# Kernel tuning notes

Hardware: AMD Instinct MI355X
Metric: run time of the kernel (lower is better)

Reference implementation:

```python
import jax, jax.numpy as jnp
import numpy as np

N = 128  # image size
J = 4    # number of scales
L = 4    # number of orientations


def make_morlet_filters(n, j_max, n_angles):
    """Fixed Morlet filter bank in Fourier space, shape [J, L, N, N] (real)."""
    freqs = np.fft.fftfreq(n) * 2.0 * np.pi
    kx = freqs[:, None] * np.ones((1, n))
    ky = np.ones((n, 1)) * freqs[None, :]
    filters = np.zeros((j_max, n_angles, n, n), dtype=np.float32)
    for j in range(j_max):
        k0 = 3.0 * np.pi / 4.0 / (2.0 ** j)   # central frequency of scale j
        sigma = 0.8 * (2.0 ** j)               # gaussian width in space
        for l in range(n_angles):
            theta = np.pi * l / n_angles
            k0x, k0y = k0 * np.cos(theta), k0 * np.sin(theta)
            beta = np.exp(-0.5 * sigma ** 2 * k0 ** 2)  # zero-mean correction
            g_shift = np.exp(-0.5 * sigma ** 2 * ((kx - k0x) ** 2 + (ky - k0y) ** 2))
            g_zero = np.exp(-0.5 * sigma ** 2 * (kx ** 2 + ky ** 2))
            filters[j, l] = g_shift - beta * g_zero
    return jnp.asarray(filters)


PSI = make_morlet_filters(N, J, L)  # fixed (non-learned) filter bank
VALID_PAIRS = [(j1, j2) for j1 in range(J) for j2 in range(J) if j2 > j1]  # 6 pairs


def setup_inputs() -> dict:
    key = jax.random.key(0)
    k1, k2, k3, k4, k5 = jax.random.split(key, 5)
    B = 64
    return {
        "image_batch": jax.random.normal(k1, (B, N, N), dtype=jnp.float32),
        "fc1_w": jax.random.normal(k2, (4, 11), dtype=jnp.float32) * 0.3,
        "fc1_b": jax.random.normal(k3, (4,), dtype=jnp.float32) * 0.1,
        "fc2_w": jax.random.normal(k4, (10, 4), dtype=jnp.float32) * 0.3,
        "fc2_b": jax.random.normal(k5, (10,), dtype=jnp.float32) * 0.1,
    }


def _scattering(image):
    # image: [B, N, N]
    i_hat = jnp.fft.fft2(image)  # [B,N,N] complex64
    s0 = jnp.mean(image, axis=(1, 2))  # [B]
    # first order: |x * psi_{j1,l1}|  -> [B,J,L,N,N]
    u1 = jnp.abs(jnp.fft.ifft2(i_hat[:, None, None] * PSI[None]))
    s1 = jnp.mean(u1, axis=(2, 3, 4))  # [B,J] averaged over orientations+space
    u1_hat = jnp.fft.fft2(u1)  # [B,J,L,N,N]
    # second order: only j2 > j1 (others NaN in original and masked out)
    s2_list = []
    for (j1, j2) in VALID_PAIRS:
        # [B, L1, L2, N, N]
        field = jnp.fft.ifft2(u1_hat[:, j1, :, None] * PSI[j2][None, None])
        s2_list.append(jnp.mean(jnp.abs(field), axis=(1, 2, 3, 4)))
    s2 = jnp.stack(s2_list, axis=1)  # [B,6]
    return jnp.concatenate([s0[:, None], s1, s2], axis=1)  # [B,11]


def reference(image_batch, fc1_w, fc1_b, fc2_w, fc2_b):
    coeffs = _scattering(image_batch)                      # [B,11]
    h = jax.nn.relu(coeffs @ fc1_w.T + fc1_b)              # [B,4]
    return jax.nn.sigmoid(h @ fc2_w.T + fc2_b)             # [B,10]
```

## Files before the change

### kernel.cpp

```cpp
#include <hip/hip_runtime.h>
#include <math.h>

#define NN   128
#define SS   129
#define TT   512
#define NPIX 16384
#define EPT  32
#define SG   65
#define SG32 33


__device__ __forceinline__ float2 cmul(float2 a, float2 w) {
    return make_float2(a.x * w.x - a.y * w.y, a.x * w.y + a.y * w.x);
}
__device__ __forceinline__ float2 cmulc(float2 a, float2 w) {
    return make_float2(a.x * w.x + a.y * w.y, a.y * w.x - a.x * w.y);
}

template<int SGN>
__device__ __forceinline__ void fft4(float2* f) {
    float2 t0 = make_float2(f[0].x + f[2].x, f[0].y + f[2].y);
    float2 t1 = make_float2(f[0].x - f[2].x, f[0].y - f[2].y);
    float2 t2 = make_float2(f[1].x + f[3].x, f[1].y + f[3].y);
    float2 t3 = make_float2(f[1].x - f[3].x, f[1].y - f[3].y);
    float2 t3i = (SGN > 0) ? make_float2(-t3.y, t3.x) : make_float2(t3.y, -t3.x);
    f[0] = make_float2(t0.x + t2.x, t0.y + t2.y);
    f[1] = make_float2(t1.x + t3i.x, t1.y + t3i.y);
    f[2] = make_float2(t0.x - t2.x, t0.y - t2.y);
    f[3] = make_float2(t1.x - t3i.x, t1.y - t3i.y);
}

template<int SGN>
__device__ __forceinline__ void fft8(float2* f) {
    const float R = 0.70710678118654752f;
    const float WC[4] = {1.f, R, 0.f, -R};
    const float WS[4] = {0.f, R, 1.f, R};
    #pragma unroll
    for (int stage = 0; stage < 3; ++stage) {
        const int L = 8 >> stage, half = L >> 1, step = 1 << stage;
        #pragma unroll
        for (int base = 0; base < 8; base += L) {
            #pragma unroll
            for (int j = 0; j < half; ++j) {
                float2 u = f[base + j], v = f[base + half + j];
                f[base + j] = make_float2(u.x + v.x, u.y + v.y);
                float dx = u.x - v.x, dy = u.y - v.y;
                const int t = j * step;
                const float wr = WC[t];
                const float wi = (SGN > 0) ? WS[t] : -WS[t];
                f[base + half + j] = make_float2(dx * wr - dy * wi, dx * wi + dy * wr);
            }
        }
    }
    float2 tmp;
    tmp = f[1]; f[1] = f[4]; f[4] = tmp;
    tmp = f[3]; f[3] = f[6]; f[6] = tmp;
}

template<int SGN>
__device__ __forceinline__ void fft16(float2* f) {
    const float WC[8] = {1.f, 0.92387953251f, 0.70710678119f, 0.38268343236f,
                         0.f, -0.38268343236f, -0.70710678119f, -0.92387953251f};
    const float WS[8] = {0.f, 0.38268343236f, 0.70710678119f, 0.92387953251f,
                         1.f, 0.92387953251f, 0.70710678119f, 0.38268343236f};
    #pragma unroll
    for (int stage = 0; stage < 4; ++stage) {
        const int L = 16 >> stage, half = L >> 1, step = 1 << stage;
        #pragma unroll
        for (int base = 0; base < 16; base += L) {
            #pragma unroll
            for (int j = 0; j < half; ++j) {
                float2 u = f[base + j], v = f[base + half + j];
                f[base + j] = make_float2(u.x + v.x, u.y + v.y);
                float dx = u.x - v.x, dy = u.y - v.y;
                const int t = j * step;
                const float wr = WC[t];
                const float wi = (SGN > 0) ? WS[t] : -WS[t];
                f[base + half + j] = make_float2(dx * wr - dy * wi, dx * wi + dy * wr);
            }
        }
    }
    float2 tmp;
    tmp = f[1];  f[1]  = f[8];  f[8]  = tmp;
    tmp = f[2];  f[2]  = f[4];  f[4]  = tmp;
    tmp = f[3];  f[3]  = f[12]; f[12] = tmp;
    tmp = f[5];  f[5]  = f[10]; f[10] = tmp;
    tmp = f[7];  f[7]  = f[14]; f[14] = tmp;
    tmp = f[11]; f[11] = f[13]; f[13] = tmp;
}

__device__ __forceinline__ float waveReduceSum(float v) {
    #pragma unroll
    for (int off = 32; off > 0; off >>= 1) v += __shfl_down(v, off, 64);
    return v;
}

__device__ __forceinline__ void buildTw(float2* tw, int tid) {
    if (tid < 128) {
        float s, c;
        __sincosf((float)tid * 0.04908738521234052f, &s, &c);
        tw[tid] = make_float2(c, s);
    }
}

template<int ES, int LS>
__device__ __forceinline__ void fwdA(float2* __restrict__ F,
                                     const float2* __restrict__ tw, int tid) {
    #pragma unroll
    for (int i = 0; i < 4; ++i) {
        int u = i * TT + tid;
        int t = u >> 7, x = u & 127;
        float2* M = F + x * LS;
        float2 f[8];
        #pragma unroll
        for (int n1 = 0; n1 < 8; ++n1) f[n1] = M[(t + 16 * n1) * ES];
        fft8<-1>(f);
        #pragma unroll
        for (int ka = 0; ka < 8; ++ka)
            M[(t + 16 * ka) * ES] = cmulc(f[ka], tw[t * ka]);
    }
}

template<int ES, int LS>
__device__ __forceinline__ void fwdB(float2* __restrict__ F, int tid) {
    #pragma unroll
    for (int i = 0; i < 2; ++i) {
        int u = i * TT + tid;
        int ka = u >> 7, x = u & 127;
        float2* M = F + x * LS;
        float2 g[16];
        #pragma unroll
        for (int t = 0; t < 16; ++t) g[t] = M[(16 * ka + t) * ES];
        fft16<-1>(g);
        #pragma unroll
        for (int kb = 0; kb < 16; ++kb) M[(16 * ka + kb) * ES] = g[kb];
    }
}

__device__ __forceinline__ void fwdB_col_capture(const float2* __restrict__ F, int tid,
                                                 float2* __restrict__ uh) {
    #pragma unroll
    for (int i = 0; i < 2; ++i) {
        int u = i * TT + tid;
        int ka = u >> 7, c = u & 127;
        float2 g[16];
        #pragma unroll
        for (int t = 0; t < 16; ++t) g[t] = F[(16 * ka + t) * SS + c];
        fft16<-1>(g);
        #pragma unroll
        for (int kb = 0; kb < 16; ++kb) uh[i * 16 + kb] = g[kb];
    }
}

template<int ES, int LS>
__device__ __forceinline__ void invA(float2* __restrict__ F,
                                     const float2* __restrict__ tw, int tid) {
    #pragma unroll
    for (int i = 0; i < 2; ++i) {
        int u = i * TT + tid;
        int ka = u >> 7, x = u & 127;
        float2* M = F + x * LS;
        float2 g[16];
        #pragma unroll
        for (int kb = 0; kb < 16; ++kb) g[kb] = M[(16 * ka + kb) * ES];
        fft16<1>(g);
        #pragma unroll
        for (int t = 0; t < 16; ++t)
            M[(16 * ka + t) * ES] = cmul(g[t], tw[t * ka]);
    }
}

template<int ES, int LS>
__device__ __forceinline__ void invB(float2* __restrict__ F, int tid) {
    #pragma unroll
    for (int i = 0; i < 4; ++i) {
        int u = i * TT + tid;
        int t = u >> 7, x = u & 127;
        float2* M = F + x * LS;
        float2 f[8];
        #pragma unroll
        for (int ka = 0; ka < 8; ++ka) f[ka] = M[(16 * ka + t) * ES];
        fft8<1>(f);
        #pragma unroll
        for (int nh = 0; nh < 8; ++nh) M[(t + 16 * nh) * ES] = f[nh];
    }
}

__device__ __forceinline__ void invBmag_fwdA_row(float2* __restrict__ F,
                                                 const float2* __restrict__ tw,
                                                 int tid, float& acc) {
    #pragma unroll
    for (int i = 0; i < 4; ++i) {
        int u = i * TT + tid;
        int t = u >> 7, x = u & 127;
        float2* M = F + x * SS;
        float2 f[8];
        #pragma unroll
        for (int ka = 0; ka < 8; ++ka) f[ka] = M[16 * ka + t];
        fft8<1>(f);
        #pragma unroll
        for (int nh = 0; nh < 8; ++nh) {
            float m = sqrtf(f[nh].x * f[nh].x + f[nh].y * f[nh].y);
            acc += m;
            f[nh] = make_float2(m, 0.f);
        }
        fft8<-1>(f);
        #pragma unroll
        for (int ka = 0; ka < 8; ++ka)
            M[t + 16 * ka] = cmulc(f[ka], tw[t * ka]);
    }
}

__global__ __attribute__((amdgpu_flat_work_group_size(TT, TT), amdgpu_waves_per_eu(2, 2)))
void k_pre(const float* __restrict__ img,
           float* __restrict__ psi,
           float2* __restrict__ ihat,
           float* __restrict__ coeffs) {
    __shared__ float2 F[NN * SS];
    __shared__ float2 tw[128];
    __shared__ float red[TT / 64];
    int blk = blockIdx.x, tid = threadIdx.x;
    if (blk >= 64) {
        if (blk == 80) {
            for (int i = tid; i < 64 * 11; i += TT)
                if (i % 11 != 0) coeffs[i] = 0.f;
            return;
        }
        int f = blk - 64;
        int j = f >> 2, l = f & 3;
        float k0    = 2.35619449019234493f / (float)(1 << j);
        float sigma = 0.8f * (float)(1 << j);
        float s2    = sigma * sigma;
        float theta = 0.78539816339744831f * (float)l;
        float k0x = k0 * cosf(theta);
        float k0y = k0 * sinf(theta);
        float beta = expf(-0.5f * s2 * k0 * k0);
        const float FSTEP = 0.04908738521234052f;
        float* dst = psi + (size_t)f * NPIX;
        for (int i = tid; i < NPIX; i += TT) {
            int pr = i >> 7, pc = i & 127;
            int kr = (pr >> 4) + 8 * (pr & 15);
            int kc = (pc >> 4) + 8 * (pc & 15);
            float fr = (float)(kr < 64 ? kr : kr - 128) * FSTEP;
            float fc = (float)(kc < 64 ? kc : kc - 128) * FSTEP;
            float dx = fr - k0x, dy = fc - k0y;
            float g1 = expf(-0.5f * s2 * (dx * dx + dy * dy));
            float g0 = expf(-0.5f * s2 * (fr * fr + fc * fc));
            dst[i] = g1 - beta * g0;
        }
        return;
    }
    int b = blk;
    buildTw(tw, tid);
    const float* im = img + (size_t)b * NPIX;
    float acc = 0.f;
    #pragma unroll
    for (int k = 0; k < EPT; ++k) {
        int e = k * TT + tid;
        float v = im[e];
        acc += v;
        F[(e >> 7) * SS + (e & 127)] = make_float2(v, 0.f);
    }
    float ws = waveReduceSum(acc);
    if ((tid & 63) == 0) red[tid >> 6] = ws;
    __syncthreads();
    if (tid == 0) {
        float t = 0.f;
        #pragma unroll
        for (int w = 0; w < TT / 64; ++w) t += red[w];
        coeffs[b * 11 + 0] = t * (1.f / 16384.f);
    }
    fwdA<1, SS>(F, tw, tid);  __syncthreads();
    fwdB<1, SS>(F, tid);      __syncthreads();
    fwdA<SS, 1>(F, tw, tid);  __syncthreads();
    float2 uh[32];
    fwdB_col_capture(F, tid, uh);
    float2* dst = ihat + (size_t)b * NPIX;
    #pragma unroll
    for (int i = 0; i < 2; ++i) {
        int u = i * TT + tid;
        int ka = u >> 7, c = u & 127;
        #pragma unroll
        for (int kb = 0; kb < 16; ++kb)
            dst[(16 * ka + kb) * NN + c] = uh[i * 16 + kb];
    }
}

__global__ __attribute__((amdgpu_flat_work_group_size(TT, TT), amdgpu_waves_per_eu(2, 2)))
void k_scat_big(const float2* __restrict__ ihat,
                const float* __restrict__ psi,
                float* __restrict__ coeffs) {
    __shared__ __align__(16) float2 F[16640];
    __shared__ float2 tw[128];
    float4* G4a = (float4*)F;
    float4* G4b = (float4*)(F + 8320);
    float2* G2a = F;
    float2* G2b = F + 4160;
    float2* G2c = F + 8320;
    float2* G2d = F + 12480;
    int tid = threadIdx.x;
    int x = blockIdx.x;
    int b = x & 63, l1 = x >> 6;
    const float2* ih = ihat + (size_t)b * NPIX;
    const float*  p1 = psi + (size_t)l1 * NPIX;
    buildTw(tw, tid);

    const float S1_128 = 9.3132257461547852e-10f;
    const float S2TR   = 5.6843418860808015e-14f;

    int kalo = tid >> 7, c = tid & 127;
    {
        #pragma unroll
        for (int i = 0; i < 2; ++i) {
            int ka = kalo + 4 * i;
            float2 g[16];
            #pragma unroll
            for (int kb = 0; kb < 16; ++kb) {
                int e = (16 * ka + kb) * NN + c;
                float2 z = ih[e];
                float  p = p1[e];
                g[kb] = make_float2(z.x * p, z.y * p);
            }
            fft16<1>(g);
            #pragma unroll
            for (int t = 0; t < 16; ++t)
                F[(16 * ka + t) * SS + c] = cmul(g[t], tw[t * ka]);
        }
    }
    __syncthreads();
    invB<SS, 1>(F, tid);      __syncthreads();
    invA<1, SS>(F, tw, tid);  __syncthreads();
    float acc = 0.f;
    invBmag_fwdA_row(F, tw, tid, acc);
    float ws1 = waveReduceSum(acc);
    if ((tid & 63) == 0) atomicAdd(&coeffs[b * 11 + 1], ws1 * S1_128);
    __syncthreads();
    fwdB<1, SS>(F, tid);      __syncthreads();
    fwdA<SS, 1>(F, tw, tid);  __syncthreads();
    float2 uh[32];
    fwdB_col_capture(F, tid, uh);
    __syncthreads();

    int m = c & 15;
    bool colKeep = (m < 4) || (m >= 12);
    int pc64 = 8 * (c >> 4) + ((m < 4) ? m : (m - 8));

    {
        const int ORW[4] = {21, 15, 0, -15};
        const int OCW[4] = { 0, 15, 21,  15};
        int fc = (c >> 4) + 8 * (c & 15);
        bool ckw[4]; int pcw[4];
        #pragma unroll
        for (int w = 0; w < 4; ++w) {
            int dc = (fc - OCW[w]) & 127;
            ckw[w] = (dc < 32) || (dc >= 96);
            int uc = (dc < 32) ? dc : (dc - 64);
            pcw[w] = 8 * (uc & 7) + (uc >> 3);
        }
        #pragma unroll
        for (int i = 0; i < 2; ++i) {
            int ka = kalo + 4 * i;
            #pragma unroll
            for (int kb = 0; kb < 16; ++kb) {
                int fr = ka + 8 * kb;
                float2 z = uh[i * 16 + kb];
                int e = (16 * ka + kb) * NN + c;
                #pragma unroll
                for (int w = 0; w < 4; ++w) {
                    if (ckw[w]) {
                        int dr = (fr - ORW[w]) & 127;
                        if (dr < 32 || dr >= 96) {
                            int ur = (dr < 32) ? dr : (dr - 64);
                            int pr = 8 * (ur & 7) + (ur >> 3);
                            float pv = psi[(size_t)(4 + w) * NPIX + e];
                            float2* G = (w == 0) ? G2a : (w == 1) ? G2b
                                       : (w == 2) ? G2c : G2d;
                            G[pr * SG + pcw[w]] = make_float2(z.x * pv, z.y * pv);
                        }
                    }
                }
            }
        }
        __syncthreads();
        {
            int col = tid & 63, k8 = tid >> 6;
            float2 f0[8], f1[8], f2[8], f3[8];
            #pragma unroll
            for (int kb = 0; kb < 8; ++kb) {
                int o = (8 * k8 + kb) * SG + col;
                f0[kb] = G2a[o]; f1[kb] = G2b[o]; f2[kb] = G2c[o]; f3[kb] = G2d[o];
            }
            fft8<1>(f0); fft8<1>(f1); fft8<1>(f2); fft8<1>(f3);
            #pragma unroll
            for (int q = 0; q < 8; ++q) {
                float2 w = tw[2 * q * k8];
                int o = (8 * k8 + q) * SG + col;
                G2a[o] = cmul(f0[q], w); G2b[o] = cmul(f1[q], w);
                G2c[o] = cmul(f2[q], w); G2d[o] = cmul(f3[q], w);
            }
        }
        __syncthreads();
        {
            int col = tid & 63, q = tid >> 6;
            float2 f0[8], f1[8], f2[8], f3[8];
            #pragma unroll
            for (int k8 = 0; k8 < 8; ++k8) {
                int o = (8 * k8 + q) * SG + col;
                f0[k8] = G2a[o]; f1[k8] = G2b[o]; f2[k8] = G2c[o]; f3[k8] = G2d[o];
            }
            fft8<1>(f0); fft8<1>(f1); fft8<1>(f2); fft8<1>(f3);
            #pragma unroll
            for (int n1 = 0; n1 < 8; ++n1) {
                int o = (8 * n1 + q) * SG + col;
                G2a[o] = f0[n1]; G2b[o] = f1[n1]; G2c[o] = f2[n1]; G2d[o] = f3[n1];
            }
        }
        __syncthreads();
        {
            int row = tid & 63, k8 = tid >> 6;
            int base = row * SG + 8 * k8;
            float2 f0[8], f1[8], f2[8], f3[8];
            #pragma unroll
            for (int kb = 0; kb < 8; ++kb) {
                f0[kb] = G2a[base + kb]; f1[kb] = G2b[base + kb];
                f2[kb] = G2c[base + kb]; f3[kb] = G2d[base + kb];
            }
            fft8<1>(f0); fft8<1>(f1); fft8<1>(f2); fft8<1>(f3);
            #pragma unroll
            for (int q = 0; q < 8; ++q) {
                float2 w = tw[2 * q * k8];
                G2a[base + q] = cmul(f0[q], w); G2b[base + q] = cmul(f1[q], w);
                G2c[base + q] = cmul(f2[q], w); G2d[base + q] = cmul(f3[q], w);
            }
        }
        __syncthreads();
        float a2 = 0.f;
        {
            int row = tid & 63, q = tid >> 6;
            int base = row * SG + q;
            float2 f0[8], f1[8], f2[8], f3[8];
            #pragma unroll
            for (int k8 = 0; k8 < 8; ++k8) {
                int o = base + 8 * k8;
                f0[k8] = G2a[o]; f1[k8] = G2b[o]; f2[k8] = G2c[o]; f3[k8] = G2d[o];
            }
            fft8<1>(f0); fft8<1>(f1); fft8<1>(f2); fft8<1>(f3);
            #pragma unroll
            for (int n1 = 0; n1 < 8; ++n1) {
                a2 += sqrtf(f0[n1].x * f0[n1].x + f0[n1].y * f0[n1].y);
                a2 += sqrtf(f1[n1].x * f1[n1].x + f1[n1].y * f1[n1].y);
                a2 += sqrtf(f2[n1].x * f2[n1].x + f2[n1].y * f2[n1].y);
                a2 += sqrtf(f3[n1].x * f3[n1].x + f3[n1].y * f3[n1].y);
            }
        }
        float ws2 = waveReduceSum(a2);
        if ((tid & 63) == 0) atomicAdd(&coeffs[b * 11 + 5 + 0], ws2 * S2TR);
        __syncthreads();
    }

    for (int j2 = 2; j2 <= 3; ++j2) {
        int pair = j2 - 1;
        const float* p0 = psi + (size_t)(j2 * 4 + 0) * NPIX;
        const float* pq1 = p0 + NPIX;
        const float* pq2 = pq1 + NPIX;
        const float* pq3 = pq2 + NPIX;
        if (colKeep) {
            #pragma unroll
            for (int i = 0; i < 2; ++i) {
                int ka = kalo + 4 * i;
                #pragma unroll
                for (int kb = 0; kb < 16; ++kb) {
                    if (kb < 4 || kb >= 12) {
                        int pr64 = 8 * ka + ((kb < 4) ? kb : (kb - 8));
                        float2 z = uh[i * 16 + kb];
                        int e = (16 * ka + kb) * NN + c;
                        float a0 = p0[e], a1 = pq1[e], a2f = pq2[e], a3 = pq3[e];
                        G4a[pr64 * SG + pc64] =
                            make_float4(z.x * a0, z.y * a0, z.x * a1, z.y * a1);
                        G4b[pr64 * SG + pc64] =
                            make_float4(z.x * a2f, z.y * a2f, z.x * a3, z.y * a3);
                    }
                }
            }
        }
        __syncthreads();
        {
            int col = tid & 63, k8 = tid >> 6;
            float2 f0[8], f1[8], f2[8], f3[8];
            #pragma unroll
            for (int kb = 0; kb < 8; ++kb) {
                int o = (8 * k8 + kb) * SG + col;
                float4 v = G4a[o];
                f0[kb] = make_float2(v.x, v.y); f1[kb] = make_float2(v.z, v.w);
                float4 u = G4b[o];
                f2[kb] = make_float2(u.x, u.y); f3[kb] = make_float2(u.z, u.w);
            }
            fft8<1>(f0); fft8<1>(f1); fft8<1>(f2); fft8<1>(f3);
            #pragma unroll
            for (int q = 0; q < 8; ++q) {
                float2 w = tw[2 * q * k8];
                int o = (8 * k8 + q) * SG + col;
                float2 a = cmul(f0[q], w), d = cmul(f1[q], w);
                G4a[o] = make_float4(a.x, a.y, d.x, d.y);
                float2 a2c = cmul(f2[q], w), d2 = cmul(f3[q], w);
                G4b[o] = make_float4(a2c.x, a2c.y, d2.x, d2.y);
            }
        }
        __syncthreads();
        {
            int col = tid & 63, q = tid >> 6;
            float2 f0[8], f1[8], f2[8], f3[8];
            #pragma unroll
            for (int k8 = 0; k8 < 8; ++k8) {
                int o = (8 * k8 + q) * SG + col;
                float4 v = G4a[o];
                f0[k8] = make_float2(v.x, v.y); f1[k8] = make_float2(v.z, v.w);
                float4 u = G4b[o];
                f2[k8] = make_float2(u.x, u.y); f3[k8] = make_float2(u.z, u.w);
            }
            fft8<1>(f0); fft8<1>(f1); fft8<1>(f2); fft8<1>(f3);
            #pragma unroll
            for (int n1 = 0; n1 < 8; ++n1) {
                int o = (8 * n1 + q) * SG + col;
                G4a[o] = make_float4(f0[n1].x, f0[n1].y, f1[n1].x, f1[n1].y);
                G4b[o] = make_float4(f2[n1].x, f2[n1].y, f3[n1].x, f3[n1].y);
            }
        }
        __syncthreads();
        {
            int row = tid & 63, k8 = tid >> 6;
            int base = row * SG + 8 * k8;
            float2 f0[8], f1[8], f2[8], f3[8];
            #pragma unroll
            for (int kb = 0; kb < 8; ++kb) {
                float4 v = G4a[base + kb];
                f0[kb] = make_float2(v.x, v.y); f1[kb] = make_float2(v.z, v.w);
                float4 u = G4b[base + kb];
                f2[kb] = make_float2(u.x, u.y); f3[kb] = make_float2(u.z, u.w);
            }
            fft8<1>(f0); fft8<1>(f1); fft8<1>(f2); fft8<1>(f3);
            #pragma unroll
            for (int q = 0; q < 8; ++q) {
                float2 w = tw[2 * q * k8];
                float2 a = cmul(f0[q], w), d = cmul(f1[q], w);
                G4a[base + q] = make_float4(a.x, a.y, d.x, d.y);
                float2 a2c = cmul(f2[q], w), d2 = cmul(f3[q], w);
                G4b[base + q] = make_float4(a2c.x, a2c.y, d2.x, d2.y);
            }
        }
        __syncthreads();
        float a2 = 0.f;
        {
            int row = tid & 63, q = tid >> 6;
            int base = row * SG + q;
            float2 f0[8], f1[8], f2[8], f3[8];
            #pragma unroll
            for (int k8 = 0; k8 < 8; ++k8) {
                float4 v = G4a[base + 8 * k8];
                f0[k8] = make_float2(v.x, v.y); f1[k8] = make_float2(v.z, v.w);
                float4 u = G4b[base + 8 * k8];
                f2[k8] = make_float2(u.x, u.y); f3[k8] = make_float2(u.z, u.w);
            }
            fft8<1>(f0); fft8<1>(f1); fft8<1>(f2); fft8<1>(f3);
            #pragma unroll
            for (int n1 = 0; n1 < 8; ++n1) {
                a2 += sqrtf(f0[n1].x * f0[n1].x + f0[n1].y * f0[n1].y);
                a2 += sqrtf(f1[n1].x * f1[n1].x + f1[n1].y * f1[n1].y);
                a2 += sqrtf(f2[n1].x * f2[n1].x + f2[n1].y * f2[n1].y);
                a2 += sqrtf(f3[n1].x * f3[n1].x + f3[n1].y * f3[n1].y);
            }
        }
        float ws2 = waveReduceSum(a2);
        if ((tid & 63) == 0) atomicAdd(&coeffs[b * 11 + 5 + pair], ws2 * S2TR);
        __syncthreads();
    }
}

__global__ __attribute__((amdgpu_flat_work_group_size(TT, TT), amdgpu_waves_per_eu(4, 4)))
void k_scat_small(const float2* __restrict__ ihat,
                  const float* __restrict__ psi,
                  float* __restrict__ coeffs) {
    __shared__ __align__(16) float2 S[8320];
    __shared__ float2 tw[128];
    float2* G2  = S;
    float2* G32 = S;
    float4* G32p = (float4*)S;
    float4* G4  = (float4*)S;
    float2* H32 = S + 4160;
    int tid = threadIdx.x;
    int x = blockIdx.x;
    int b = x & 63, l1 = (x >> 6) & 3;
    int t0 = x >> 8;
    int j1 = (t0 == 0) ? 1 : (t0 + 1);
    const float2* ih = ihat + (size_t)b * NPIX;
    const float*  p1 = psi + (size_t)(j1 * 4 + l1) * NPIX;
    buildTw(tw, tid);

    const float S1_64 = 3.7252902984619141e-9f;
    const float S1_32 = 1.4901161193847656e-8f;
    const float S2_32 = 9.0949470177292824e-13f;
    const float S2_V  = 2.2737367544323206e-13f;

    int kalo = tid >> 7, c = tid & 127;

    if (t0 == 0) {
        const int OR1[4] = {21, 15, 0, -15};
        const int OC1[4] = { 0, 15, 21,  15};
        int fc = (c >> 4) + 8 * (c & 15);
        int dc = (fc - OC1[l1]) & 127;
        bool ck = (dc < 32) || (dc >= 96);
        int ucw = (dc < 32) ? dc : (dc - 64);
        int pcd = 8 * (ucw & 7) + (ucw >> 3);
        if (ck) {
            #pragma unroll
            for (int i = 0; i < 2; ++i) {
                int ka = kalo + 4 * i;
                #pragma unroll
                for (int kb = 0; kb < 16; ++kb) {
                    int fr = ka + 8 * kb;
                    int dr = (fr - OR1[l1]) & 127;
                    if (dr < 32 || dr >= 96) {
                        int ur = (dr < 32) ? dr : (dr - 64);
                        int pr = 8 * (ur & 7) + (ur >> 3);
                        int e = (16 * ka + kb) * NN + c;
                        float2 z = ih[e];
                        float  p = p1[e];
                        G2[pr * SG + pcd] = make_float2(z.x * p, z.y * p);
                    }
                }
            }
        }
        __syncthreads();
        {
            int col = tid & 63, k8 = tid >> 6;
            float2 f[8];
            #pragma unroll
            for (int kb = 0; kb < 8; ++kb) f[kb] = G2[(8 * k8 + kb) * SG + col];
            fft8<1>(f);
            #pragma unroll
            for (int q = 0; q < 8; ++q)
                G2[(8 * k8 + q) * SG + col] = cmul(f[q], tw[2 * q * k8]);
        }
        __syncthreads();
        {
            int col = tid & 63, q = tid >> 6;
            float2 f[8];
            #pragma unroll
            for (int k8 = 0; k8 < 8; ++k8) f[k8] = G2[(8 * k8 + q) * SG + col];
            fft8<1>(f);
            #pragma unroll
            for (int n1 = 0; n1 < 8; ++n1) G2[(8 * n1 + q) * SG + col] = f[n1];
        }
        __syncthreads();
        {
            int row = tid & 63, k8 = tid >> 6;
            float2* R = G2 + row * SG + 8 * k8;
            float2 f[8];
            #pragma unroll
            for (int kb = 0; kb < 8; ++kb) f[kb] = R[kb];
            fft8<1>(f);
            #pragma unroll
            for (int q = 0; q < 8; ++q) R[q] = cmul(f[q], tw[2 * q * k8]);
        }
        __syncthreads();
        float acc = 0.f;
        {
            int row = tid & 63, q = tid >> 6;
            float2* R = G2 + row * SG + q;
            float2 f[8];
            #pragma unroll
            for (int k8 = 0; k8 < 8; ++k8) f[k8] = R[8 * k8];
            fft8<1>(f);
            #pragma unroll
            for (int n1 = 0; n1 < 8; ++n1) {
                float mg = sqrtf(f[n1].x * f[n1].x + f[n1].y * f[n1].y);
                acc += mg;
                f[n1] = make_float2(mg, 0.f);
            }
            fft8<-1>(f);
            #pragma unroll
            for (int ka = 0; ka < 8; ++ka)
                R[8 * ka] = cmulc(f[ka], tw[2 * q * ka]);
        }
        float ws1 = waveReduceSum(acc);
        if ((tid & 63) == 0) atomicAdd(&coeffs[b * 11 + 2], ws1 * S1_64);
        __syncthreads();
        {
            int row2 = tid & 63, ka = tid >> 6;
            float2* R2 = G2 + row2 * SG + 8 * ka;
            float2 g[8];
            #pragma unroll
            for (int t = 0; t < 8; ++t) g[t] = R2[t];
            fft8<-1>(g);
            #pragma unroll
            for (int kb = 0; kb < 8; ++kb) R2[kb] = g[kb];
        }
        __syncthreads();
        {
            int col = tid & 63, t = tid >> 6;
            float2 g[8];
            #pragma unroll
            for (int n1 = 0; n1 < 8; ++n1) g[n1] = G2[(t + 8 * n1) * SG + col];
            fft8<-1>(g);
            #pragma unroll
            for (int ka = 0; ka < 8; ++ka)
                G2[(t + 8 * ka) * SG + col] = cmulc(g[ka], tw[2 * t * ka]);
        }
        __syncthreads();
        float2 vh[8];
        int c6 = tid & 63, ka8 = tid >> 6;
        {
            float2 g[8];
            #pragma unroll
            for (int t = 0; t < 8; ++t) g[t] = G2[(8 * ka8 + t) * SG + c6];
            fft8<-1>(g);
            #pragma unroll
            for (int kb = 0; kb < 8; ++kb) vh[kb] = g[kb];
        }
        __syncthreads();

        int uc64 = 8 * (c6 & 7) + (c6 >> 3);
        int fc128 = (uc64 < 32) ? uc64 : (uc64 + 64);
        int scI = 16 * (fc128 & 7) + (fc128 >> 3);
        int se[8];
        #pragma unroll
        for (int kb = 0; kb < 8; ++kb) {
            int ur = 8 * kb + ka8;
            int fr128 = (ur < 32) ? ur : (ur + 64);
            se[kb] = (16 * (fr128 & 7) + (fr128 >> 3)) * NN + scI;
        }

        for (int j2 = 2; j2 <= 3; ++j2) {
            int pair = j2 + 1;
            for (int half = 0; half < 2; ++half) {
                const float* p2a = psi + (size_t)(j2 * 4 + 2 * half) * NPIX;
                const float* p2b = p2a + NPIX;
                #pragma unroll
                for (int kb = 0; kb < 8; ++kb) {
                    float pa = p2a[se[kb]], pb = p2b[se[kb]];
                    G4[(8 * ka8 + kb) * SG + c6] =
                        make_float4(vh[kb].x * pa, vh[kb].y * pa,
                                    vh[kb].x * pb, vh[kb].y * pb);
                }
                __syncthreads();
                {
                    int col = tid & 63, k8 = tid >> 6;
                    float2 f0[8], f1[8];
                    #pragma unroll
                    for (int kb = 0; kb < 8; ++kb) {
                        float4 v = G4[(8 * k8 + kb) * SG + col];
                        f0[kb] = make_float2(v.x, v.y); f1[kb] = make_float2(v.z, v.w);
                    }
                    fft8<1>(f0); fft8<1>(f1);
                    #pragma unroll
                    for (int q = 0; q < 8; ++q) {
                        float2 w = tw[2 * q * k8];
                        float2 a = cmul(f0[q], w), d = cmul(f1[q], w);
                        G4[(8 * k8 + q) * SG + col] = make_float4(a.x, a.y, d.x, d.y);
                    }
                }
                __syncthreads();
                {
                    int col = tid & 63, q = tid >> 6;
                    float2 f0[8], f1[8];
                    #pragma unroll
                    for (int k8 = 0; k8 < 8; ++k8) {
                        float4 v = G4[(8 * k8 + q) * SG + col];
                        f0[k8] = make_float2(v.x, v.y); f1[k8] = make_float2(v.z, v.w);
                    }
                    fft8<1>(f0); fft8<1>(f1);
                    #pragma unroll
                    for (int n1 = 0; n1 < 8; ++n1)
                        G4[(8 * n1 + q) * SG + col] =
                            make_float4(f0[n1].x, f0[n1].y, f1[n1].x, f1[n1].y);
                }
                __syncthreads();
                {
                    int row = tid & 63, k8 = tid >> 6;
                    float4* R = G4 + row * SG + 8 * k8;
                    float2 f0[8], f1[8];
                    #pragma unroll
                    for (int kb = 0; kb < 8; ++kb) {
                        float4 v = R[kb];
                        f0[kb] = make_float2(v.x, v.y); f1[kb] = make_float2(v.z, v.w);
                    }
                    fft8<1>(f0); fft8<1>(f1);
                    #pragma unroll
                    for (int q = 0; q < 8; ++q) {
                        float2 w = tw[2 * q * k8];
                        float2 a = cmul(f0[q], w), d = cmul(f1[q], w);
                        R[q] = make_float4(a.x, a.y, d.x, d.y);
                    }
                }
                __syncthreads();
                float a2 = 0.f;
                {
                    int row = tid & 63, q = tid >> 6;
                    float4* R = G4 + row * SG + q;
                    float2 f0[8], f1[8];
                    #pragma unroll
                    for (int k8 = 0; k8 < 8; ++k8) {
                        float4 v = R[8 * k8];
                        f0[k8] = make_float2(v.x, v.y); f1[k8] = make_float2(v.z, v.w);
                    }
                    fft8<1>(f0); fft8<1>(f1);
                    #pragma unroll
                    for (int n1 = 0; n1 < 8; ++n1) {
                        a2 += sqrtf(f0[n1].x * f0[n1].x + f0[n1].y * f0[n1].y);
                        a2 += sqrtf(f1[n1].x * f1[n1].x + f1[n1].y * f1[n1].y);
                    }
                }
                float ws2 = waveReduceSum(a2);
                if ((tid & 63) == 0) atomicAdd(&coeffs[b * 11 + 5 + pair], ws2 * S2_V);
                __syncthreads();
            }
        }
        return;
    }

    if (t0 == 2) {
        int m = c & 15;
        bool ck32 = (m < 2) || (m >= 14);
        int pc32 = 4 * (c >> 4) + ((m < 2) ? m : (m - 12));
        if (ck32) {
            #pragma unroll
            for (int i = 0; i < 2; ++i) {
                int ka = kalo + 4 * i;
                #pragma unroll
                for (int kb = 0; kb < 16; ++kb) {
                    if (kb < 2 || kb >= 14) {
                        int e = (16 * ka + kb) * NN + c;
                        float2 z = ih[e];
                        float  p = p1[e];
                        int pr32 = 4 * ka + ((kb < 2) ? kb : (kb - 12));
                        G32[pr32 * SG32 + pc32] = make_float2(z.x * p, z.y * p);
                    }
                }
            }
        }
        __syncthreads();
        if (tid < 256) {
            int line = tid & 31, a = tid >> 5;
            float2 f[4];
            #pragma unroll
            for (int kb = 0; kb < 4; ++kb) f[kb] = G32[(4 * a + kb) * SG32 + line];
            fft4<1>(f);
            #pragma unroll
            for (int t = 0; t < 4; ++t)
                G32[(4 * a + t) * SG32 + line] = cmul(f[t], tw[4 * t * a]);
        }
        __syncthreads();
        if (tid < 128) {
            int line = tid & 31, t = tid >> 5;
            float2 f[8];
            #pragma unroll
            for (int a = 0; a < 8; ++a) f[a] = G32[(4 * a + t) * SG32 + line];
            fft8<1>(f);
            #pragma unroll
            for (int n1 = 0; n1 < 8; ++n1) G32[(4 * n1 + t) * SG32 + line] = f[n1];
        }
        __syncthreads();
        if (tid < 256) {
            int row = tid & 31, a = tid >> 5;
            float2* R = G32 + row * SG32 + 4 * a;
            float2 f[4];
            #pragma unroll
            for (int kb = 0; kb < 4; ++kb) f[kb] = R[kb];
            fft4<1>(f);
            #pragma unroll
            for (int t = 0; t < 4; ++t) R[t] = cmul(f[t], tw[4 * t * a]);
        }
        __syncthreads();
        float acc = 0.f;
        if (tid < 128) {
            int row = tid & 31, t = tid >> 5;
            float2* R = G32 + row * SG32 + t;
            float2 f[8];
            #pragma unroll
            for (int a = 0; a < 8; ++a) f[a] = R[4 * a];
            fft8<1>(f);
            #pragma unroll
            for (int n1 = 0; n1 < 8; ++n1)
                acc += sqrtf(f[n1].x * f[n1].x + f[n1].y * f[n1].y);
        }
        float ws1 = waveReduceSum(acc);
        if ((tid & 63) == 0 && tid < 128) atomicAdd(&coeffs[b * 11 + 4], ws1 * S1_32);
        return;
    }

    int m = c & 15;
    bool colKeep = (m < 4) || (m >= 12);
    if (colKeep) {
        #pragma unroll
        for (int i = 0; i < 2; ++i) {
            int ka = kalo + 4 * i;
            #pragma unroll
            for (int kb = 0; kb < 16; ++kb) {
                if (kb < 4 || kb >= 12) {
                    int e = (16 * ka + kb) * NN + c;
                    float2 z = ih[e];
                    float  p = p1[e];
                    int pr64 = 8 * ka + ((kb < 4) ? kb : (kb - 8));
                    int pc64 = 8 * (c >> 4) + ((m < 4) ? m : (m - 8));
                    G2[pr64 * SG + pc64] = make_float2(z.x * p, z.y * p);
                }
            }
        }
    }
    __syncthreads();
    {
        int col = tid & 63, k8 = tid >> 6;
        float2 f[8];
        #pragma unroll
        for (int kb = 0; kb < 8; ++kb) f[kb] = G2[(8 * k8 + kb) * SG + col];
        fft8<1>(f);
        #pragma unroll
        for (int q = 0; q < 8; ++q)
            G2[(8 * k8 + q) * SG + col] = cmul(f[q], tw[2 * q * k8]);
    }
    __syncthreads();
    {
        int col = tid & 63, q = tid >> 6;
        float2 f[8];
        #pragma unroll
        for (int k8 = 0; k8 < 8; ++k8) f[k8] = G2[(8 * k8 + q) * SG + col];
        fft8<1>(f);
        #pragma unroll
        for (int n1 = 0; n1 < 8; ++n1) G2[(8 * n1 + q) * SG + col] = f[n1];
    }
    __syncthreads();
    {
        int row = tid & 63, k8 = tid >> 6;
        float2* R = G2 + row * SG + 8 * k8;
        float2 f[8];
        #pragma unroll
        for (int kb = 0; kb < 8; ++kb) f[kb] = R[kb];
        fft8<1>(f);
        #pragma unroll
        for (int q = 0; q < 8; ++q) R[q] = cmul(f[q], tw[2 * q * k8]);
    }
    __syncthreads();
    float acc = 0.f;
    {
        int row = tid & 63, q = tid >> 6;
        float2* R = G2 + row * SG + q;
        float2 f[8];
        #pragma unroll
        for (int k8 = 0; k8 < 8; ++k8) f[k8] = R[8 * k8];
        fft8<1>(f);
        #pragma unroll
        for (int n1 = 0; n1 < 8; ++n1) {
            float mg = sqrtf(f[n1].x * f[n1].x + f[n1].y * f[n1].y);
            acc += mg;
            f[n1] = make_float2(mg, 0.f);
        }
        fft8<-1>(f);
        #pragma unroll
        for (int ka = 0; ka < 8; ++ka)
            R[8 * ka] = cmulc(f[ka], tw[2 * q * ka]);
    }
    float ws1 = waveReduceSum(acc);
    if ((tid & 63) == 0) atomicAdd(&coeffs[b * 11 + 3], ws1 * S1_64);
    __syncthreads();
    {
        int row2 = tid & 63, ka = tid >> 6;
        float2* R2 = G2 + row2 * SG + 8 * ka;
        float2 g[8];
        #pragma unroll
        for (int t = 0; t < 8; ++t) g[t] = R2[t];
        fft8<-1>(g);
        #pragma unroll
        for (int kb = 0; kb < 8; ++kb) R2[kb] = g[kb];
    }
    __syncthreads();
    {
        int col = tid & 63, t = tid >> 6;
        float2 g[8];
        #pragma unroll
        for (int n1 = 0; n1 < 8; ++n1) g[n1] = G2[(t + 8 * n1) * SG + col];
        fft8<-1>(g);
        #pragma unroll
        for (int ka = 0; ka < 8; ++ka)
            G2[(t + 8 * ka) * SG + col] = cmulc(g[ka], tw[2 * t * ka]);
    }
    __syncthreads();
    {
        int col = tid & 63, ka = tid >> 6;
        float2 g[8];
        #pragma unroll
        for (int t = 0; t < 8; ++t) g[t] = G2[(8 * ka + t) * SG + col];
        fft8<-1>(g);
        int br = col & 7, ar = col >> 3;
        if (br < 2 || br >= 6) {
            int p32row = 4 * ar + (br & 3);
            #pragma unroll
            for (int kb = 0; kb < 8; ++kb) {
                if (kb < 2 || kb >= 6)
                    H32[(4 * ka + (kb & 3)) * 32 + p32row] = g[kb];
            }
        }
    }
    __syncthreads();

    bool ck32 = (m < 2) || (m >= 14);
    int pc32 = 4 * (c >> 4) + ((m < 2) ? m : (m - 12));
    for (int half = 0; half < 2; ++half) {
        const float* p2a = psi + (size_t)(12 + 2 * half) * NPIX;
        const float* p2b = p2a + NPIX;
        if (ck32) {
            #pragma unroll
            for (int i = 0; i < 2; ++i) {
                int ka = kalo + 4 * i;
                #pragma unroll
                for (int kb = 0; kb < 16; ++kb) {
                    if (kb < 2 || kb >= 14) {
                        int pr32 = 4 * ka + ((kb < 2) ? kb : (kb - 12));
                        float2 z = H32[pr32 * 32 + pc32];
                        int e = (16 * ka + kb) * NN + c;
                        float pa = p2a[e], pb = p2b[e];
                        G32p[pr32 * SG32 + pc32] =
                            make_float4(z.x * pa, z.y * pa, z.x * pb, z.y * pb);
                    }
                }
            }
        }
        __syncthreads();
        if (tid < 256) {
            int line = tid & 31, a = tid >> 5;
            float2 f0[4], f1[4];
            #pragma unroll
            for (int kb = 0; kb < 4; ++kb) {
                float4 v = G32p[(4 * a + kb) * SG32 + line];
                f0[kb] = make_float2(v.x, v.y); f1[kb] = make_float2(v.z, v.w);
            }
            fft4<1>(f0); fft4<1>(f1);
            #pragma unroll
            for (int t = 0; t < 4; ++t) {
                float2 w = tw[4 * t * a];
                float2 aa = cmul(f0[t], w), d = cmul(f1[t], w);
                G32p[(4 * a + t) * SG32 + line] = make_float4(aa.x, aa.y, d.x, d.y);
            }
        }
        __syncthreads();
        if (tid < 128) {
            int line = tid & 31, t = tid >> 5;
            float2 f0[8], f1[8];
            #pragma unroll
            for (int a = 0; a < 8; ++a) {
                float4 v = G32p[(4 * a + t) * SG32 + line];
                f0[a] = make_float2(v.x, v.y); f1[a] = make_float2(v.z, v.w);
            }
            fft8<1>(f0); fft8<1>(f1);
            #pragma unroll
            for (int n1 = 0; n1 < 8; ++n1)
                G32p[(4 * n1 + t) * SG32 + line] =
                    make_float4(f0[n1].x, f0[n1].y, f1[n1].x, f1[n1].y);
        }
        __syncthreads();
        if (tid < 256) {
            int row = tid & 31, a = tid >> 5;
            float4* R = G32p + row * SG32 + 4 * a;
            float2 f0[4], f1[4];
            #pragma unroll
            for (int kb = 0; kb < 4; ++kb) {
                float4 v = R[kb];
                f0[kb] = make_float2(v.x, v.y); f1[kb] = make_float2(v.z, v.w);
            }
            fft4<1>(f0); fft4<1>(f1);
            #pragma unroll
            for (int t = 0; t < 4; ++t) {
                float2 w = tw[4 * t * a];
                float2 aa = cmul(f0[t], w), d = cmul(f1[t], w);
                R[t] = make_float4(aa.x, aa.y, d.x, d.y);
            }
        }
        __syncthreads();
        float a2 = 0.f;
        if (tid < 128) {
            int row = tid & 31, t = tid >> 5;
            float4* R = G32p + row * SG32 + t;
            float2 f0[8], f1[8];
            #pragma unroll
            for (int a = 0; a < 8; ++a) {
                float4 v = R[4 * a];
                f0[a] = make_float2(v.x, v.y); f1[a] = make_float2(v.z, v.w);
            }
            fft8<1>(f0); fft8<1>(f1);
            #pragma unroll
            for (int n1 = 0; n1 < 8; ++n1) {
                a2 += sqrtf(f0[n1].x * f0[n1].x + f0[n1].y * f0[n1].y);
                a2 += sqrtf(f1[n1].x * f1[n1].x + f1[n1].y * f1[n1].y);
            }
        }
        float ws2 = waveReduceSum(a2);
        if ((tid & 63) == 0 && tid < 128)
            atomicAdd(&coeffs[b * 11 + 5 + 5], ws2 * S2_32);
        __syncthreads();
    }
}

__global__ void k_mlp(const float* __restrict__ coeffs,
                      const float* __restrict__ w1, const float* __restrict__ b1,
                      const float* __restrict__ w2, const float* __restrict__ b2,
                      float* __restrict__ out) {
    int b = threadIdx.x;
    if (b >= 64) return;
    float c[11];
    #pragma unroll
    for (int i = 0; i < 11; ++i) c[i] = coeffs[b * 11 + i];
    float h[4];
    #pragma unroll
    for (int k = 0; k < 4; ++k) {
        float s = b1[k];
        #pragma unroll
        for (int i = 0; i < 11; ++i) s += w1[k * 11 + i] * c[i];
        h[k] = fmaxf(s, 0.f);
    }
    #pragma unroll
    for (int o = 0; o < 10; ++o) {
        float s = b2[o];
        #pragma unroll
        for (int k = 0; k < 4; ++k) s += w2[o * 4 + k] * h[k];
        out[b * 10 + o] = 1.f / (1.f + expf(-s));
    }
}

extern "C" void kernel_launch(void* const* d_in, const int* in_sizes, int n_in,
                              void* d_out, int out_size, void* d_ws, size_t ws_size,
                              hipStream_t stream) {
    const float* img = (const float*)d_in[0];
    const float* w1  = (const float*)d_in[1];
    const float* b1  = (const float*)d_in[2];
    const float* w2  = (const float*)d_in[3];
    const float* b2  = (const float*)d_in[4];
    float* out = (float*)d_out;

    float*  ws     = (float*)d_ws;
    float*  psi    = ws;
    float2* ihat   = (float2*)(ws + 16 * NPIX);
    float*  coeffs = ws + 16 * NPIX + 2 * 64 * NPIX;

    hipLaunchKernelGGL(k_pre,        dim3(81),  dim3(TT), 0, stream, img, psi, ihat, coeffs);
    hipLaunchKernelGGL(k_scat_big,   dim3(256), dim3(TT), 0, stream, ihat, psi, coeffs);
    hipLaunchKernelGGL(k_scat_small, dim3(768), dim3(TT), 0, stream, ihat, psi, coeffs);
    hipLaunchKernelGGL(k_mlp,        dim3(1),   dim3(64), 0, stream, coeffs, w1, b1, w2, b2, out);
}
```

Before: 198.5 us.

## Run j2=3 second-order pairs at 32x32 with all four orientations per pass

Adds a shared helper that computes four orientation products of a cropped 32x32 spectrum at once, splitting them across two LDS buffers so all 512 threads take part in the radix passes. The j2=3 pairs, previously computed with wider 64-point or two half passes, now use this 32x32 band-limited path in both kernels. This removes one of the two passes and some larger-FFT work, on the premise that the j2=3 filter is negligible outside the 32x32 band. The cost is more LDS space, and accuracy now depends on that band-limit holding.

```diff
diff --git a/kernel.cpp b/kernel.cpp
--- a/kernel.cpp
+++ b/kernel.cpp
@@ -101,6 +101,84 @@
         __sincosf((float)tid * 0.04908738521234052f, &s, &c);
         tw[tid] = make_float2(c, s);
     }
+}
+
+__device__ __forceinline__ float pass32x4(float4* __restrict__ P4a,
+                                          float4* __restrict__ P4b,
+                                          const float2* __restrict__ tw, int tid) {
+    __syncthreads();
+    {
+        float4* P = (tid & 256) ? P4b : P4a;
+        int line = tid & 31, a = (tid >> 5) & 7;
+        float2 f0[4], f1[4];
+        #pragma unroll
+        for (int kb = 0; kb < 4; ++kb) {
+            float4 v = P[(4 * a + kb) * SG32 + line];
+            f0[kb] = make_float2(v.x, v.y); f1[kb] = make_float2(v.z, v.w);
+        }
+        fft4<1>(f0); fft4<1>(f1);
+        #pragma unroll
+        for (int t = 0; t < 4; ++t) {
+            float2 w = tw[4 * t * a];
+            float2 aa = cmul(f0[t], w), d = cmul(f1[t], w);
+            P[(4 * a + t) * SG32 + line] = make_float4(aa.x, aa.y, d.x, d.y);
+        }
+    }
+    __syncthreads();
+    if (tid < 256) {
+        float4* P = (tid & 128) ? P4b : P4a;
+        int line = tid & 31, t = (tid >> 5) & 3;
+        float2 f0[8], f1[8];
+        #pragma unroll
+        for (int a = 0; a < 8; ++a) {
+            float4 v = P[(4 * a + t) * SG32 + line];
+            f0[a] = make_float2(v.x, v.y); f1[a] = make_float2(v.z, v.w);
+        }
+        fft8<1>(f0); fft8<1>(f1);
+        #pragma unroll
+        for (int n1 = 0; n1 < 8; ++n1)
+            P[(4 * n1 + t) * SG32 + line] =
+                make_float4(f0[n1].x, f0[n1].y, f1[n1].x, f1[n1].y);
+    }
+    __syncthreads();
+    {
+        float4* P = (tid & 256) ? P4b : P4a;
+        int row = tid & 31, a = (tid >> 5) & 7;
+        float4* R = P + row * SG32 + 4 * a;
+        float2 f0[4], f1[4];
+        #pragma unroll
+        for (int kb = 0; kb < 4; ++kb) {
+            float4 v = R[kb];
+            f0[kb] = make_float2(v.x, v.y); f1[kb] = make_float2(v.z, v.w);
+        }
+        fft4<1>(f0); fft4<1>(f1);
+        #pragma unroll
+        for (int t = 0; t < 4; ++t) {
+            float2 w = tw[4 * t * a];
+            float2 aa = cmul(f0[t], w), d = cmul(f1[t], w);
+            R[t] = make_float4(aa.x, aa.y, d.x, d.y);
+        }
+    }
+    __syncthreads();
+    float a2 = 0.f;
+    if (tid < 256) {
+        float4* P = (tid & 128) ? P4b : P4a;
+        int row = tid & 31, t = (tid >> 5) & 3;
+        float4* R = P + row * SG32 + t;
+        float2 f0[8], f1[8];
+        #pragma unroll
+        for (int a = 0; a < 8; ++a) {
+            float4 v = R[4 * a];
+            f0[a] = make_float2(v.x, v.y); f1[a] = make_float2(v.z, v.w);
+        }
+        fft8<1>(f0); fft8<1>(f1);
+        #pragma unroll
+        for (int n1 = 0; n1 < 8; ++n1) {
+            a2 += sqrtf(f0[n1].x * f0[n1].x + f0[n1].y * f0[n1].y);
+            a2 += sqrtf(f1[n1].x * f1[n1].x + f1[n1].y * f1[n1].y);
+        }
+    }
+    return a2;
 }
 
 template<int ES, int LS>
@@ -298,6 +376,8 @@
     float2* G2b = F + 4160;
     float2* G2c = F + 8320;
     float2* G2d = F + 12480;
+    float4* P4a = (float4*)F;
+    float4* P4b = (float4*)F + 1056;
     int tid = threadIdx.x;
     int x = blockIdx.x;
     int b = x & 63, l1 = x >> 6;
@@ -307,6 +387,7 @@
 
     const float S1_128 = 9.3132257461547852e-10f;
     const float S2TR   = 5.6843418860808015e-14f;
+    const float S2_03  = 2.2737367544323206e-13f;
 
     int kalo = tid >> 7, c = tid & 127;
     {
@@ -458,9 +539,8 @@
         __syncthreads();
     }
 
-    for (int j2 = 2; j2 <= 3; ++j2) {
-        int pair = j2 - 1;
-        const float* p0 = psi + (size_t)(j2 * 4 + 0) * NPIX;
+    {
+        const float* p0 = psi + (size_t)8 * NPIX;
         const float* pq1 = p0 + NPIX;
         const float* pq2 = pq1 + NPIX;
         const float* pq3 = pq2 + NPIX;
@@ -571,8 +651,39 @@
             }
         }
         float ws2 = waveReduceSum(a2);
-        if ((tid & 63) == 0) atomicAdd(&coeffs[b * 11 + 5 + pair], ws2 * S2TR);
-        __syncthreads();
+        if ((tid & 63) == 0) atomicAdd(&coeffs[b * 11 + 5 + 1], ws2 * S2TR);
+        __syncthreads();
+    }
+
+    {
+        bool ck32 = (m < 2) || (m >= 14);
+        int pc32 = 4 * (c >> 4) + ((m < 2) ? m : (m - 12));
+        const float* p0 = psi + (size_t)12 * NPIX;
+        const float* pq1 = p0 + NPIX;
+        const float* pq2 = pq1 + NPIX;
+        const float* pq3 = pq2 + NPIX;
+        if (ck32) {
+            #pragma unroll
+            for (int i = 0; i < 2; ++i) {
+                int ka = kalo + 4 * i;
+                #pragma unroll
+                for (int kb = 0; kb < 16; ++kb) {
+                    if (kb < 2 || kb >= 14) {
+                        int pr32 = 4 * ka + ((kb < 2) ? kb : (kb - 12));
+                        float2 z = uh[i * 16 + kb];
+                        int e = (16 * ka + kb) * NN + c;
+                        float a0 = p0[e], a1 = pq1[e], a2f = pq2[e], a3 = pq3[e];
+                        P4a[pr32 * SG32 + pc32] =
+                            make_float4(z.x * a0, z.y * a0, z.x * a1, z.y * a1);
+                        P4b[pr32 * SG32 + pc32] =
+                            make_float4(z.x * a2f, z.y * a2f, z.x * a3, z.y * a3);
+                    }
+                }
+            }
+        }
+        float a2 = pass32x4(P4a, P4b, tw, tid);
+        float ws2 = waveReduceSum(a2);
+        if ((tid & 63) == 0) atomicAdd(&coeffs[b * 11 + 5 + 2], ws2 * S2_03);
     }
 }
 
@@ -584,9 +695,10 @@
     __shared__ float2 tw[128];
     float2* G2  = S;
     float2* G32 = S;
-    float4* G32p = (float4*)S;
     float4* G4  = (float4*)S;
-    float2* H32 = S + 4160;
+    float4* P4a = (float4*)S;
+    float4* P4b = (float4*)S + 1056;
+    float2* H32 = S + 6144;
     int tid = threadIdx.x;
     int x = blockIdx.x;
     int b = x & 63, l1 = (x >> 6) & 3;
@@ -730,10 +842,9 @@
             se[kb] = (16 * (fr128 & 7) + (fr128 >> 3)) * NN + scI;
         }
 
-        for (int j2 = 2; j2 <= 3; ++j2) {
-            int pair = j2 + 1;
+        {
             for (int half = 0; half < 2; ++half) {
-                const float* p2a = psi + (size_t)(j2 * 4 + 2 * half) * NPIX;
+                const float* p2a = psi + (size_t)(8 + 2 * half) * NPIX;
                 const float* p2b = p2a + NPIX;
                 #pragma unroll
                 for (int kb = 0; kb < 8; ++kb) {
@@ -811,9 +922,37 @@
                     }
                 }
                 float ws2 = waveReduceSum(a2);
-                if ((tid & 63) == 0) atomicAdd(&coeffs[b * 11 + 5 + pair], ws2 * S2_V);
+                if ((tid & 63) == 0) atomicAdd(&coeffs[b * 11 + 5 + 3], ws2 * S2_V);
                 __syncthreads();
             }
+        }
+
+        {
+            int m6 = c6 & 7;
+            bool ckV = (m6 < 2) || (m6 >= 6);
+            int p32c = 4 * (c6 >> 3) + ((m6 < 2) ? m6 : (m6 - 4));
+            const float* p0 = psi + (size_t)12 * NPIX;
+            const float* pq1 = p0 + NPIX;
+            const float* pq2 = pq1 + NPIX;
+            const float* pq3 = pq2 + NPIX;
+            if (ckV) {
+                #pragma unroll
+                for (int kb = 0; kb < 8; ++kb) {
+                    if (kb < 2 || kb >= 6) {
+                        int pr32 = 4 * ka8 + (kb & 3);
+                        float2 z = vh[kb];
+                        float a0 = p0[se[kb]], a1 = pq1[se[kb]];
+                        float a2f = pq2[se[kb]], a3 = pq3[se[kb]];
+                        P4a[pr32 * SG32 + p32c] =
+                            make_float4(z.x * a0, z.y * a0, z.x * a1, z.y * a1);
+                        P4b[pr32 * SG32 + p32c] =
+                            make_float4(z.x * a2f, z.y * a2f, z.x * a3, z.y * a3);
+                    }
+                }
+            }
+            float a2 = pass32x4(P4a, P4b, tw, tid);
+            float ws2 = waveReduceSum(a2);
+            if ((tid & 63) == 0) atomicAdd(&coeffs[b * 11 + 5 + 4], ws2 * S2_32);
         }
         return;
     }
@@ -1002,11 +1141,13 @@
     }
     __syncthreads();
 
-    bool ck32 = (m < 2) || (m >= 14);
-    int pc32 = 4 * (c >> 4) + ((m < 2) ? m : (m - 12));
-    for (int half = 0; half < 2; ++half) {
-        const float* p2a = psi + (size_t)(12 + 2 * half) * NPIX;
-        const float* p2b = p2a + NPIX;
+    {
+        bool ck32 = (m < 2) || (m >= 14);
+        int pc32 = 4 * (c >> 4) + ((m < 2) ? m : (m - 12));
+        const float* p0 = psi + (size_t)12 * NPIX;
+        const float* pq1 = p0 + NPIX;
+        const float* pq2 = pq1 + NPIX;
+        const float* pq3 = pq2 + NPIX;
         if (ck32) {
             #pragma unroll
             for (int i = 0; i < 2; ++i) {
@@ -1017,85 +1158,18 @@
                         int pr32 = 4 * ka + ((kb < 2) ? kb : (kb - 12));
                         float2 z = H32[pr32 * 32 + pc32];
                         int e = (16 * ka + kb) * NN + c;
-                        float pa = p2a[e], pb = p2b[e];
-                        G32p[pr32 * SG32 + pc32] =
-                            make_float4(z.x * pa, z.y * pa, z.x * pb, z.y * pb);
+                        float a0 = p0[e], a1 = pq1[e], a2f = pq2[e], a3 = pq3[e];
+                        P4a[pr32 * SG32 + pc32] =
+                            make_float4(z.x * a0, z.y * a0, z.x * a1, z.y * a1);
+                        P4b[pr32 * SG32 + pc32] =
+                            make_float4(z.x * a2f, z.y * a2f, z.x * a3, z.y * a3);
                     }
                 }
             }
         }
-        __syncthreads();
-        if (tid < 256) {
-            int line = tid & 31, a = tid >> 5;
-            float2 f0[4], f1[4];
-            #pragma unroll
-            for (int kb = 0; kb < 4; ++kb) {
-                float4 v = G32p[(4 * a + kb) * SG32 + line];
-                f0[kb] = make_float2(v.x, v.y); f1[kb] = make_float2(v.z, v.w);
-            }
-            fft4<1>(f0); fft4<1>(f1);
-            #pragma unroll
-            for (int t = 0; t < 4; ++t) {
-                float2 w = tw[4 * t * a];
-                float2 aa = cmul(f0[t], w), d = cmul(f1[t], w);
-                G32p[(4 * a + t) * SG32 + line] = make_float4(aa.x, aa.y, d.x, d.y);
-            }
-        }
-        __syncthreads();
-        if (tid < 128) {
-            int line = tid & 31, t = tid >> 5;
-            float2 f0[8], f1[8];
-            #pragma unroll
-            for (int a = 0; a < 8; ++a) {
-                float4 v = G32p[(4 * a + t) * SG32 + line];
-                f0[a] = make_float2(v.x, v.y); f1[a] = make_float2(v.z, v.w);
-            }
-            fft8<1>(f0); fft8<1>(f1);
-            #pragma unroll
-            for (int n1 = 0; n1 < 8; ++n1)
-                G32p[(4 * n1 + t) * SG32 + line] =
-                    make_float4(f0[n1].x, f0[n1].y, f1[n1].x, f1[n1].y);
-        }
-        __syncthreads();
-        if (tid < 256) {
-            int row = tid & 31, a = tid >> 5;
-            float4* R = G32p + row * SG32 + 4 * a;
-            float2 f0[4], f1[4];
-            #pragma unroll
-            for (int kb = 0; kb < 4; ++kb) {
-                float4 v = R[kb];
-                f0[kb] = make_float2(v.x, v.y); f1[kb] = make_float2(v.z, v.w);
-            }
-            fft4<1>(f0); fft4<1>(f1);
-            #pragma unroll
-            for (int t = 0; t < 4; ++t) {
-                float2 w = tw[4 * t * a];
-                float2 aa = cmul(f0[t], w), d = cmul(f1[t], w);
-                R[t] = make_float4(aa.x, aa.y, d.x, d.y);
-            }
-        }
-        __syncthreads();
-        float a2 = 0.f;
-        if (tid < 128) {
-            int row = tid & 31, t = tid >> 5;
-            float4* R = G32p + row * SG32 + t;
-            float2 f0[8], f1[8];
-            #pragma unroll
-            for (int a = 0; a < 8; ++a) {
-                float4 v = R[4 * a];
-                f0[a] = make_float2(v.x, v.y); f1[a] = make_float2(v.z, v.w);
-            }
-            fft8<1>(f0); fft8<1>(f1);
-            #pragma unroll
-            for (int n1 = 0; n1 < 8; ++n1) {
-                a2 += sqrtf(f0[n1].x * f0[n1].x + f0[n1].y * f0[n1].y);
-                a2 += sqrtf(f1[n1].x * f1[n1].x + f1[n1].y * f1[n1].y);
-            }
-        }
+        float a2 = pass32x4(P4a, P4b, tw, tid);
         float ws2 = waveReduceSum(a2);
-        if ((tid & 63) == 0 && tid < 128)
-            atomicAdd(&coeffs[b * 11 + 5 + 5], ws2 * S2_32);
-        __syncthreads();
+        if ((tid & 63) == 0) atomicAdd(&coeffs[b * 11 + 5 + 5], ws2 * S2_32);
     }
 }
 
```

New measurement: 184.5 us. -7.0%, faster.
